# Optimization experiments

Hardware: AMD Instinct MI355X
Metric: run time of the kernel (lower is better)

Reference implementation:

```python
import jax, jax.numpy as jnp
import numpy as np

B, N, D, K, H = 32768, 17, 2, 3, 64


def _mlp_params(key, n, d_in, d_hid, d_out):
    k1, k2, k3, k4 = jax.random.split(key, 4)
    W1 = jax.random.normal(k1, (n, d_in, d_hid), jnp.float32) / np.sqrt(d_in)
    b1 = jnp.zeros((n, d_hid), jnp.float32)
    W2 = jax.random.normal(k2, (n, d_hid, d_out), jnp.float32) / np.sqrt(d_hid)
    b2 = jnp.zeros((n, d_out), jnp.float32)
    return W1, b1, W2, b2


def setup_inputs() -> dict:
    key = jax.random.key(0)
    kp, kk, kw, kb = jax.random.split(key, 4)
    pred_pts = jax.random.normal(kp, (B, N, D), jnp.float32)
    kW1, kb1, kW2, kb2 = _mlp_params(kk, N, D, H, K)            # k_nets
    wW1, wb1, wW2, wb2 = _mlp_params(kw, N, D, H, K)            # weight_nets
    bW1, bb1, bW2, bb2 = _mlp_params(kb, N, D, 2 * H, K * 2 * D)  # basis_nets
    return dict(pred_pts=pred_pts,
                kW1=kW1, kb1=kb1, kW2=kW2, kb2=kb2,
                wW1=wW1, wb1=wb1, wW2=wW2, wb2=wb2,
                bW1=bW1, bb1=bb1, bW2=bW2, bb2=bb2)


def _per_joint_mlp(x, W1, b1, W2, b2):
    # x: [B,N,D]; W1: [N,D,Hd]; W2: [N,Hd,O]
    h = jax.nn.relu(jnp.einsum('bnd,ndh->bnh', x, W1) + b1[None])
    return jnp.einsum('bnh,nho->bno', h, W2) + b2[None]


def reference(pred_pts, kW1, kb1, kW2, kb2, wW1, wb1, wW2, wb2, bW1, bb1, bW2, bb2):
    Bc, Nc, Dc = pred_pts.shape
    Kc = kW2.shape[-1]

    # k-selection head (eval mode: argmax, +1)
    k_logits = _per_joint_mlp(pred_pts, kW1, kb1, kW2, kb2)      # [B,N,K]
    k_js = jnp.argmax(k_logits, axis=-1) + 1                     # [B,N] int

    # mixture weights
    w = jax.nn.softmax(_per_joint_mlp(pred_pts, wW1, wb1, wW2, wb2), axis=-1)  # [B,N,K]

    # basis parameters: mu, sigma = exp(log_sigma)
    params = _per_joint_mlp(pred_pts, bW1, bb1, bW2, bb2).reshape(Bc, Nc, Kc, 2 * Dc)
    mu = params[..., :Dc]                                         # [B,N,K,D]
    sigma = jnp.exp(params[..., Dc:])                             # [B,N,K,D]

    # top-k selection by descending weight (indices are constants w.r.t. grad)
    idx = jnp.argsort(-w, axis=-1)                                # [B,N,K]
    mu_top = jnp.take_along_axis(mu, idx[..., None], axis=2)      # [B,N,K,D]
    sigma_top = jnp.take_along_axis(sigma, idx[..., None], axis=2)
    mask = jnp.arange(Kc)[None, None, :] < k_js[..., None]        # [B,N,K] bool

    # pack float outputs: weights + selected (mu, sigma) -> [B,N,K,1+2D]
    out = jnp.concatenate([w[..., None], mu_top, sigma_top], axis=-1)
    return out, k_js, mask
```

## Files before the change

kernel.cpp:

```cpp
#include <hip/hip_runtime.h>
#include <cmath>

#define NBATCH 32768
#define NJOINT 17
#define OUT0_ELEMS (NBATCH * NJOINT * 15)
#define KJS_OFF    OUT0_ELEMS
#define MASK_OFF   (KJS_OFF + NBATCH * NJOINT)

#define WN_STRIDE 774
#define WS_DOUBLES (NJOINT * WN_STRIDE)

__device__ __forceinline__ float sel3f(int i, float a, float b, float c) {
    return (i == 0) ? a : ((i == 1) ? b : c);
}

__global__ void cvt_weights_f64(
    const float* __restrict__ kW1, const float* __restrict__ kb1,
    const float* __restrict__ kW2, const float* __restrict__ kb2,
    const float* __restrict__ wW1, const float* __restrict__ wb1,
    const float* __restrict__ wW2, const float* __restrict__ wb2,
    double* __restrict__ dws)
{
    const int n = blockIdx.x;
    double* o = dws + (size_t)n * WN_STRIDE;
    for (int i = threadIdx.x; i < WN_STRIDE; i += blockDim.x) {
        int j = i;
        const float* W1 = kW1; const float* b1 = kb1;
        const float* W2 = kW2; const float* b2 = kb2;
        if (j >= 387) { j -= 387; W1 = wW1; b1 = wb1; W2 = wW2; b2 = wb2; }
        float v;
        if (j < 128)      v = W1[n * 128 + j];
        else if (j < 192) v = b1[n * 64 + (j - 128)];
        else if (j < 384) v = W2[n * 192 + (j - 192)];
        else              v = b2[n * 3 + (j - 384)];
        o[i] = (double)v;
    }
}

__device__ __forceinline__ void mlp64_ws_2(
    const double* __restrict__ gws,
    double xA0, double xA1, double xB0, double xB1,
    double& lA0, double& lA1, double& lA2,
    double& lB0, double& lB1, double& lB2)
{
    const double* W1a = gws;
    const double* W1b = gws + 64;
    const double* b1  = gws + 128;
    const double* W2  = gws + 192;
    lA0 = gws[384]; lA1 = gws[385]; lA2 = gws[386];
    lB0 = gws[384]; lB1 = gws[385]; lB2 = gws[386];
    #pragma unroll 4
    for (int h = 0; h < 64; ++h) {
        const double wa = W1a[h], wb = W1b[h], bb = b1[h];
        const double w0 = W2[h * 3 + 0], w1 = W2[h * 3 + 1], w2 = W2[h * 3 + 2];
        double hvA = fmax(fma(xA1, wb, fma(xA0, wa, bb)), 0.0);
        double hvB = fmax(fma(xB1, wb, fma(xB0, wa, bb)), 0.0);
        lA0 = fma(hvA, w0, lA0); lB0 = fma(hvB, w0, lB0);
        lA1 = fma(hvA, w1, lA1); lB1 = fma(hvB, w1, lB1);
        lA2 = fma(hvA, w2, lA2); lB2 = fma(hvB, w2, lB2);
    }
}

__device__ __forceinline__ void mlp64_cvt_2(
    const float* __restrict__ W1, const float* __restrict__ b1f,
    const float* __restrict__ W2f, const float* __restrict__ b2f, int n,
    double xA0, double xA1, double xB0, double xB1,
    double& lA0, double& lA1, double& lA2,
    double& lB0, double& lB1, double& lB2)
{
    const float* W1a = W1 + n * 128;
    const float* W1b = W1a + 64;
    const float* b1  = b1f + n * 64;
    const float* W2  = W2f + n * 192;
    lA0 = (double)b2f[n * 3 + 0]; lB0 = lA0;
    lA1 = (double)b2f[n * 3 + 1]; lB1 = lA1;
    lA2 = (double)b2f[n * 3 + 2]; lB2 = lA2;
    #pragma unroll 4
    for (int h = 0; h < 64; ++h) {
        const double wa = (double)W1a[h], wb = (double)W1b[h], bb = (double)b1[h];
        const double w0 = (double)W2[h * 3 + 0], w1 = (double)W2[h * 3 + 1],
                     w2 = (double)W2[h * 3 + 2];
        double hvA = fmax(fma(xA1, wb, fma(xA0, wa, bb)), 0.0);
        double hvB = fmax(fma(xB1, wb, fma(xB0, wa, bb)), 0.0);
        lA0 = fma(hvA, w0, lA0); lB0 = fma(hvB, w0, lB0);
        lA1 = fma(hvA, w1, lA1); lB1 = fma(hvB, w1, lB1);
        lA2 = fma(hvA, w2, lA2); lB2 = fma(hvB, w2, lB2);
    }
}

__device__ __forceinline__ void decide(
    double kl0, double kl1, double kl2,
    double wl0, double wl1, double wl2,
    int& kj, int& i0, int& i1, int& i2,
    float& p0, float& p1, float& p2)
{
    kj = 0;
    {
        double m = kl0;
        if (kl1 > m) { m = kl1; kj = 1; }
        if (kl2 > m) { kj = 2; }
    }
    i0 = 0;
    {
        double m = wl0;
        if (wl1 > m) { m = wl1; i0 = 1; }
        if (wl2 > m) { i0 = 2; }
    }
    const int ia = (i0 == 0) ? 1 : 0;
    const int ib = (i0 == 2) ? 1 : 2;
    const double wa = ia ? wl1 : wl0;
    const double wb = (ib == 1) ? wl1 : wl2;
    i1 = (wb > wa) ? ib : ia;
    i2 = (wb > wa) ? ia : ib;

    const double mw = fmax(fmax(wl0, wl1), wl2);
    const float e0 = __expf((float)(wl0 - mw));
    const float e1 = __expf((float)(wl1 - mw));
    const float e2 = __expf((float)(wl2 - mw));
    const float inv = 1.0f / (e0 + e1 + e2);
    p0 = e0 * inv; p1 = e1 * inv; p2 = e2 * inv;
}

__device__ __forceinline__ void epilogue(
    const float acc[12], int i0, int i1, int i2,
    float p0, float p1, float p2, float r[15])
{
    r[0]  = p0; r[5] = p1; r[10] = p2;
    r[1]  = sel3f(i0, acc[0], acc[4], acc[8]);
    r[2]  = sel3f(i0, acc[1], acc[5], acc[9]);
    r[3]  = __expf(sel3f(i0, acc[2], acc[6], acc[10]));
    r[4]  = __expf(sel3f(i0, acc[3], acc[7], acc[11]));
    r[6]  = sel3f(i1, acc[0], acc[4], acc[8]);
    r[7]  = sel3f(i1, acc[1], acc[5], acc[9]);
    r[8]  = __expf(sel3f(i1, acc[2], acc[6], acc[10]));
    r[9]  = __expf(sel3f(i1, acc[3], acc[7], acc[11]));
    r[11] = sel3f(i2, acc[0], acc[4], acc[8]);
    r[12] = sel3f(i2, acc[1], acc[5], acc[9]);
    r[13] = __expf(sel3f(i2, acc[2], acc[6], acc[10]));
    r[14] = __expf(sel3f(i2, acc[3], acc[7], acc[11]));
}

template<bool USE_WS>
__device__ __forceinline__ void compute2(
    int n, float xA0f, float xA1f, float xB0f, float xB1f,
    const float* __restrict__ kW1, const float* __restrict__ kb1,
    const float* __restrict__ kW2, const float* __restrict__ kb2,
    const float* __restrict__ wW1, const float* __restrict__ wb1,
    const float* __restrict__ wW2, const float* __restrict__ wb2,
    const float* __restrict__ bW1, const float* __restrict__ bb1,
    const float* __restrict__ bW2, const float* __restrict__ bb2,
    const double* __restrict__ dws,
    float rA[15], float rB[15], int& kjA, int& kjB)
{
    const double xA0 = (double)xA0f, xA1 = (double)xA1f;
    const double xB0 = (double)xB0f, xB1 = (double)xB1f;

    double klA0, klA1, klA2, klB0, klB1, klB2;
    double wlA0, wlA1, wlA2, wlB0, wlB1, wlB2;
    if constexpr (USE_WS) {
        const double* Wn = dws + (size_t)n * WN_STRIDE;
        mlp64_ws_2(Wn,       xA0, xA1, xB0, xB1, klA0, klA1, klA2, klB0, klB1, klB2);
        mlp64_ws_2(Wn + 387, xA0, xA1, xB0, xB1, wlA0, wlA1, wlA2, wlB0, wlB1, wlB2);
    } else {
        mlp64_cvt_2(kW1, kb1, kW2, kb2, n, xA0, xA1, xB0, xB1,
                    klA0, klA1, klA2, klB0, klB1, klB2);
        mlp64_cvt_2(wW1, wb1, wW2, wb2, n, xA0, xA1, xB0, xB1,
                    wlA0, wlA1, wlA2, wlB0, wlB1, wlB2);
    }

    int i0A, i1A, i2A, i0B, i1B, i2B;
    float p0A, p1A, p2A, p0B, p1B, p2B;
    decide(klA0, klA1, klA2, wlA0, wlA1, wlA2, kjA, i0A, i1A, i2A, p0A, p1A, p2A);
    decide(klB0, klB1, klB2, wlB0, wlB1, wlB2, kjB, i0B, i1B, i2B, p0B, p1B, p2B);

    float accA[12], accB[12];
    {
        const float* W1a = bW1 + n * 256;
        const float* W1b = W1a + 128;
        const float* b1  = bb1 + n * 128;
        const float* W2  = bW2 + n * 1536;
        const float* b2  = bb2 + n * 12;
        #pragma unroll
        for (int j = 0; j < 12; ++j) { accA[j] = b2[j]; accB[j] = b2[j]; }
        #pragma unroll 4
        for (int h = 0; h < 128; ++h) {
            const float wa = W1a[h], wb = W1b[h], bb = b1[h];
            float hvA = fmaxf(fmaf(xA1f, wb, fmaf(xA0f, wa, bb)), 0.0f);
            float hvB = fmaxf(fmaf(xB1f, wb, fmaf(xB0f, wa, bb)), 0.0f);
            #pragma unroll
            for (int j = 0; j < 12; ++j) {
                const float wv = W2[h * 12 + j];
                accA[j] = fmaf(hvA, wv, accA[j]);
                accB[j] = fmaf(hvB, wv, accB[j]);
            }
        }
    }

    epilogue(accA, i0A, i1A, i2A, p0A, p1A, p2A, rA);
    epilogue(accB, i0B, i1B, i2B, p0B, p1B, p2B, rB);
}

template<bool USE_WS>
__global__ __launch_bounds__(128, 4) void mdn_fused(
    const float* __restrict__ pred_pts,
    const float* __restrict__ kW1, const float* __restrict__ kb1,
    const float* __restrict__ kW2, const float* __restrict__ kb2,
    const float* __restrict__ wW1, const float* __restrict__ wb1,
    const float* __restrict__ wW2, const float* __restrict__ wb2,
    const float* __restrict__ bW1, const float* __restrict__ bb1,
    const float* __restrict__ bW2, const float* __restrict__ bb2,
    float* __restrict__ out,
    const double* __restrict__ dws)
{
    const int l    = threadIdx.x;
    const int w    = l >> 6;
    const int lane = l & 63;
    const int bx   = blockIdx.x;
    const int by   = blockIdx.y;
    const int n0   = by * 2;

    if (by == 8 && w == 1) return;
    int n = n0 + w;
    n = __builtin_amdgcn_readfirstlane(n);

    const int bA = bx * 128 + lane;
    const int bB = bA + 64;
    const int pA = bA * NJOINT + n;
    const int pB = bB * NJOINT + n;

    const float2 xA = *reinterpret_cast<const float2*>(pred_pts + 2 * pA);
    const float2 xB = *reinterpret_cast<const float2*>(pred_pts + 2 * pB);

    float rA[15], rB[15];
    int kjA, kjB;
    compute2<USE_WS>(n, xA.x, xA.y, xB.x, xB.y,
                     kW1, kb1, kW2, kb2, wW1, wb1, wW2, wb2,
                     bW1, bb1, bW2, bb2, dws, rA, rB, kjA, kjB);

    if (by == 8) {
        float* oA = out + (size_t)pA * 15;
        float* oB = out + (size_t)pB * 15;
        #pragma unroll
        for (int i = 0; i < 15; ++i) { oA[i] = rA[i]; oB[i] = rB[i]; }
        out[KJS_OFF + pA] = (float)(kjA + 1);
        out[KJS_OFF + pB] = (float)(kjB + 1);
        float* mkA = out + MASK_OFF + (size_t)pA * 3;
        mkA[0] = 1.0f; mkA[1] = (kjA >= 1) ? 1.0f : 0.0f; mkA[2] = (kjA >= 2) ? 1.0f : 0.0f;
        float* mkB = out + MASK_OFF + (size_t)pB * 3;
        mkB[0] = 1.0f; mkB[1] = (kjB >= 1) ? 1.0f : 0.0f; mkB[2] = (kjB >= 2) ? 1.0f : 0.0f;
        return;
    }

    __shared__ float s_out[256 * 17];
    {
        float* soA = s_out + (w * 128 + lane) * 17;
        float* soB = soA + 64 * 17;
        #pragma unroll
        for (int j = 0; j < 15; ++j) { soA[j] = rA[j]; soB[j] = rB[j]; }
        soA[15] = (float)(kjA + 1);
        soB[15] = (float)(kjB + 1);
    }
    __syncthreads();

    if (l < 120) {
        const int c_off = l / 30;
        const int jj    = l - c_off * 30;
        const int nl    = jj / 15;
        const int j     = jj - nl * 15;
        const int lbase = (nl * 128 + c_off) * 17 + j;
        size_t g = (size_t)((bx * 128 + c_off) * NJOINT + n0) * 15 + jj;
        #pragma unroll
        for (int rr = 0; rr < 32; ++rr) {
            out[g] = s_out[lbase + 68 * rr];
            g += 1020;
        }
    }

    #pragma unroll
    for (int it = 0; it < 2; ++it) {
        const int q   = it * 128 + l;
        const int bl  = q >> 1;
        const int nlr = q & 1;
        const float kjf = s_out[(nlr * 128 + bl) * 17 + 15];
        const int pg = (bx * 128 + bl) * NJOINT + n0 + nlr;
        out[KJS_OFF + pg] = kjf;
        float* mk = out + MASK_OFF + (size_t)pg * 3;
        mk[0] = 1.0f;
        mk[1] = (kjf >= 1.5f) ? 1.0f : 0.0f;
        mk[2] = (kjf >= 2.5f) ? 1.0f : 0.0f;
    }
}

extern "C" void kernel_launch(void* const* d_in, const int* in_sizes, int n_in,
                              void* d_out, int out_size, void* d_ws, size_t ws_size,
                              hipStream_t stream) {
    (void)in_sizes; (void)n_in; (void)out_size;
    const bool use_ws = (d_ws != nullptr) && (ws_size >= (size_t)WS_DOUBLES * sizeof(double));
    dim3 grid(NBATCH / 128, 9);
    if (use_ws) {
        cvt_weights_f64<<<NJOINT, 256, 0, stream>>>(
            (const float*)d_in[1], (const float*)d_in[2],
            (const float*)d_in[3], (const float*)d_in[4],
            (const float*)d_in[5], (const float*)d_in[6],
            (const float*)d_in[7], (const float*)d_in[8],
            (double*)d_ws);
        mdn_fused<true><<<grid, 128, 0, stream>>>(
            (const float*)d_in[0],
            (const float*)d_in[1], (const float*)d_in[2],
            (const float*)d_in[3], (const float*)d_in[4],
            (const float*)d_in[5], (const float*)d_in[6],
            (const float*)d_in[7], (const float*)d_in[8],
            (const float*)d_in[9], (const float*)d_in[10],
            (const float*)d_in[11], (const float*)d_in[12],
            (float*)d_out, (const double*)d_ws);
    } else {
        mdn_fused<false><<<grid, 128, 0, stream>>>(
            (const float*)d_in[0],
            (const float*)d_in[1], (const float*)d_in[2],
            (const float*)d_in[3], (const float*)d_in[4],
            (const float*)d_in[5], (const float*)d_in[6],
            (const float*)d_in[7], (const float*)d_in[8],
            (const float*)d_in[9], (const float*)d_in[10],
            (const float*)d_in[11], (const float*)d_in[12],
            (float*)d_out, nullptr);
    }
}
```

Measured before the change: 142.4 us.

## Compute selection MLPs in fp32, fall back to fp64 only for near-ties

```diff
diff --git a/kernel.cpp b/kernel.cpp
--- a/kernel.cpp
+++ b/kernel.cpp
@@ -37,55 +37,77 @@
     }
 }
 
-__device__ __forceinline__ void mlp64_ws_2(
-    const double* __restrict__ gws,
-    double xA0, double xA1, double xB0, double xB1,
-    double& lA0, double& lA1, double& lA2,
-    double& lB0, double& lB1, double& lB2)
+__device__ __forceinline__ void mlp32_2(
+    const float* __restrict__ W1, const float* __restrict__ b1f,
+    const float* __restrict__ W2f, const float* __restrict__ b2f, int n,
+    float xA0, float xA1, float xB0, float xB1,
+    float& lA0, float& lA1, float& lA2,
+    float& lB0, float& lB1, float& lB2)
+{
+    const float* W1a = W1 + n * 128;
+    const float* W1b = W1a + 64;
+    const float* b1  = b1f + n * 64;
+    const float* W2  = W2f + n * 192;
+    lA0 = b2f[n * 3 + 0]; lB0 = lA0;
+    lA1 = b2f[n * 3 + 1]; lB1 = lA1;
+    lA2 = b2f[n * 3 + 2]; lB2 = lA2;
+    #pragma unroll 4
+    for (int h = 0; h < 64; ++h) {
+        const float wa = W1a[h], wb = W1b[h], bb = b1[h];
+        const float w0 = W2[h * 3 + 0], w1 = W2[h * 3 + 1], w2 = W2[h * 3 + 2];
+        float hvA = fmaxf(fmaf(xA1, wb, fmaf(xA0, wa, bb)), 0.0f);
+        float hvB = fmaxf(fmaf(xB1, wb, fmaf(xB0, wa, bb)), 0.0f);
+        lA0 = fmaf(hvA, w0, lA0); lB0 = fmaf(hvB, w0, lB0);
+        lA1 = fmaf(hvA, w1, lA1); lB1 = fmaf(hvB, w1, lB1);
+        lA2 = fmaf(hvA, w2, lA2); lB2 = fmaf(hvB, w2, lB2);
+    }
+}
+
+__device__ __forceinline__ void mlp64_ws_1(
+    const double* __restrict__ gws, double x0, double x1,
+    double& l0, double& l1, double& l2)
 {
     const double* W1a = gws;
     const double* W1b = gws + 64;
     const double* b1  = gws + 128;
     const double* W2  = gws + 192;
-    lA0 = gws[384]; lA1 = gws[385]; lA2 = gws[386];
-    lB0 = gws[384]; lB1 = gws[385]; lB2 = gws[386];
+    l0 = gws[384]; l1 = gws[385]; l2 = gws[386];
     #pragma unroll 4
     for (int h = 0; h < 64; ++h) {
-        const double wa = W1a[h], wb = W1b[h], bb = b1[h];
-        const double w0 = W2[h * 3 + 0], w1 = W2[h * 3 + 1], w2 = W2[h * 3 + 2];
-        double hvA = fmax(fma(xA1, wb, fma(xA0, wa, bb)), 0.0);
-        double hvB = fmax(fma(xB1, wb, fma(xB0, wa, bb)), 0.0);
-        lA0 = fma(hvA, w0, lA0); lB0 = fma(hvB, w0, lB0);
-        lA1 = fma(hvA, w1, lA1); lB1 = fma(hvB, w1, lB1);
-        lA2 = fma(hvA, w2, lA2); lB2 = fma(hvB, w2, lB2);
-    }
-}
-
-__device__ __forceinline__ void mlp64_cvt_2(
+        double hv = fmax(fma(x1, W1b[h], fma(x0, W1a[h], b1[h])), 0.0);
+        l0 = fma(hv, W2[h * 3 + 0], l0);
+        l1 = fma(hv, W2[h * 3 + 1], l1);
+        l2 = fma(hv, W2[h * 3 + 2], l2);
+    }
+}
+
+__device__ __forceinline__ void mlp64_cvt_1(
     const float* __restrict__ W1, const float* __restrict__ b1f,
     const float* __restrict__ W2f, const float* __restrict__ b2f, int n,
-    double xA0, double xA1, double xB0, double xB1,
-    double& lA0, double& lA1, double& lA2,
-    double& lB0, double& lB1, double& lB2)
+    double x0, double x1, double& l0, double& l1, double& l2)
 {
     const float* W1a = W1 + n * 128;
     const float* W1b = W1a + 64;
     const float* b1  = b1f + n * 64;
     const float* W2  = W2f + n * 192;
-    lA0 = (double)b2f[n * 3 + 0]; lB0 = lA0;
-    lA1 = (double)b2f[n * 3 + 1]; lB1 = lA1;
-    lA2 = (double)b2f[n * 3 + 2]; lB2 = lA2;
+    l0 = (double)b2f[n * 3 + 0];
+    l1 = (double)b2f[n * 3 + 1];
+    l2 = (double)b2f[n * 3 + 2];
     #pragma unroll 4
     for (int h = 0; h < 64; ++h) {
-        const double wa = (double)W1a[h], wb = (double)W1b[h], bb = (double)b1[h];
-        const double w0 = (double)W2[h * 3 + 0], w1 = (double)W2[h * 3 + 1],
-                     w2 = (double)W2[h * 3 + 2];
-        double hvA = fmax(fma(xA1, wb, fma(xA0, wa, bb)), 0.0);
-        double hvB = fmax(fma(xB1, wb, fma(xB0, wa, bb)), 0.0);
-        lA0 = fma(hvA, w0, lA0); lB0 = fma(hvB, w0, lB0);
-        lA1 = fma(hvA, w1, lA1); lB1 = fma(hvB, w1, lB1);
-        lA2 = fma(hvA, w2, lA2); lB2 = fma(hvB, w2, lB2);
-    }
+        double hv = fma(x1, (double)W1b[h], fma(x0, (double)W1a[h], (double)b1[h]));
+        hv = fmax(hv, 0.0);
+        l0 = fma(hv, (double)W2[h * 3 + 0], l0);
+        l1 = fma(hv, (double)W2[h * 3 + 1], l1);
+        l2 = fma(hv, (double)W2[h * 3 + 2], l2);
+    }
+}
+
+__device__ __forceinline__ bool tight3(float a, float b, float c) {
+    const float m01 = fabsf(a - b), m02 = fabsf(a - c), m12 = fabsf(b - c);
+    const float mn = fminf(m01, fminf(m02, m12));
+    const float tau = 1e-3f * (1.0f + 0.02f * (fabsf(a) + fabsf(b) + fabsf(c)));
+    return mn < tau;
 }
 
 __device__ __forceinline__ void decide(
@@ -152,20 +174,42 @@
     const double* __restrict__ dws,
     float rA[15], float rB[15], int& kjA, int& kjB)
 {
-    const double xA0 = (double)xA0f, xA1 = (double)xA1f;
-    const double xB0 = (double)xB0f, xB1 = (double)xB1f;
-
-    double klA0, klA1, klA2, klB0, klB1, klB2;
-    double wlA0, wlA1, wlA2, wlB0, wlB1, wlB2;
-    if constexpr (USE_WS) {
-        const double* Wn = dws + (size_t)n * WN_STRIDE;
-        mlp64_ws_2(Wn,       xA0, xA1, xB0, xB1, klA0, klA1, klA2, klB0, klB1, klB2);
-        mlp64_ws_2(Wn + 387, xA0, xA1, xB0, xB1, wlA0, wlA1, wlA2, wlB0, wlB1, wlB2);
-    } else {
-        mlp64_cvt_2(kW1, kb1, kW2, kb2, n, xA0, xA1, xB0, xB1,
-                    klA0, klA1, klA2, klB0, klB1, klB2);
-        mlp64_cvt_2(wW1, wb1, wW2, wb2, n, xA0, xA1, xB0, xB1,
-                    wlA0, wlA1, wlA2, wlB0, wlB1, wlB2);
+    float kA0, kA1, kA2, kB0, kB1, kB2;
+    float wA0, wA1, wA2, wB0, wB1, wB2;
+    mlp32_2(kW1, kb1, kW2, kb2, n, xA0f, xA1f, xB0f, xB1f,
+            kA0, kA1, kA2, kB0, kB1, kB2);
+    mlp32_2(wW1, wb1, wW2, wb2, n, xA0f, xA1f, xB0f, xB1f,
+            wA0, wA1, wA2, wB0, wB1, wB2);
+
+    const bool fA = tight3(kA0, kA1, kA2) || tight3(wA0, wA1, wA2);
+    const bool fB = tight3(kB0, kB1, kB2) || tight3(wB0, wB1, wB2);
+
+    double klA0 = kA0, klA1 = kA1, klA2 = kA2;
+    double klB0 = kB0, klB1 = kB1, klB2 = kB2;
+    double wlA0 = wA0, wlA1 = wA1, wlA2 = wA2;
+    double wlB0 = wB0, wlB1 = wB1, wlB2 = wB2;
+
+    if (__any(fA || fB)) {
+        if constexpr (USE_WS) {
+            const double* Wn = dws + (size_t)n * WN_STRIDE;
+            if (fA) {
+                mlp64_ws_1(Wn,       (double)xA0f, (double)xA1f, klA0, klA1, klA2);
+                mlp64_ws_1(Wn + 387, (double)xA0f, (double)xA1f, wlA0, wlA1, wlA2);
+            }
+            if (fB) {
+                mlp64_ws_1(Wn,       (double)xB0f, (double)xB1f, klB0, klB1, klB2);
+                mlp64_ws_1(Wn + 387, (double)xB0f, (double)xB1f, wlB0, wlB1, wlB2);
+            }
+        } else {
+            if (fA) {
+                mlp64_cvt_1(kW1, kb1, kW2, kb2, n, (double)xA0f, (double)xA1f, klA0, klA1, klA2);
+                mlp64_cvt_1(wW1, wb1, wW2, wb2, n, (double)xA0f, (double)xA1f, wlA0, wlA1, wlA2);
+            }
+            if (fB) {
+                mlp64_cvt_1(kW1, kb1, kW2, kb2, n, (double)xB0f, (double)xB1f, klB0, klB1, klB2);
+                mlp64_cvt_1(wW1, wb1, wW2, wb2, n, (double)xB0f, (double)xB1f, wlB0, wlB1, wlB2);
+            }
+        }
     }
 
     int i0A, i1A, i2A, i0B, i1B, i2B;
```

After: 155.7 us. 1.09x slower.
